# Optimization experiments

Measured on AMD Instinct MI355X. Metric: run time of the kernel, lower is better.

The kernel has to match this reference:

```python
import jax, jax.numpy as jnp
import numpy as np

DIL = 64  # dilation; l_wing = (filter_sz-1)*dil = 64
B, R, C, D, S, T = 8, 128, 128, 128, 256, 16384


def _xavier(key, shape, fan_in, fan_out):
    a = np.sqrt(6.0 / (fan_in + fan_out)).astype(np.float32)
    return jax.random.uniform(key, shape, jnp.float32, -a, a)


def setup_inputs() -> dict:
    key = jax.random.key(0)
    ks = jax.random.split(key, 10)
    return {
        'x': jax.random.normal(ks[0], (B, R, T), jnp.float32),
        'cond': jax.random.normal(ks[1], (B, C, T), jnp.float32),
        # dilated convs, kernel size 2: weight (out=D, in=R, k=2), bias (D,)
        'w_sig': _xavier(ks[2], (D, R, 2), R * 2, D * 2),
        'b_sig': jnp.zeros((D,), jnp.float32),
        'w_gate': _xavier(ks[3], (D, R, 2), R * 2, D * 2),
        'b_gate': jnp.zeros((D,), jnp.float32),
        # 1x1 cond projections (no bias): (D, C)
        'w_psig': _xavier(ks[4], (D, C), C, D),
        'w_pgate': _xavier(ks[5], (D, C), C, D),
        # 1x1 residual / skip projections (no bias)
        'w_res': _xavier(ks[6], (R, D), D, R),
        'w_skp': _xavier(ks[7], (S, D), D, S),
    }


def reference(x, cond, w_sig, b_sig, w_gate, b_gate, w_psig, w_pgate, w_res, w_skp):
    d = DIL
    # dilated kernel-size-2 conv1d expressed as two shifted 1x1 contractions
    x0 = x[:, :, :-d]   # tap at offset 0, length T-d
    x1 = x[:, :, d:]    # tap at offset d, length T-d
    c = cond[:, :, d:]  # cond_lead = l_wing = d in full mode
    filt = (jnp.einsum('brt,dr->bdt', x0, w_sig[:, :, 0])
            + jnp.einsum('brt,dr->bdt', x1, w_sig[:, :, 1])
            + jnp.einsum('bct,dc->bdt', c, w_psig)
            + b_sig[None, :, None])
    gate = (jnp.einsum('brt,dr->bdt', x0, w_gate[:, :, 0])
            + jnp.einsum('brt,dr->bdt', x1, w_gate[:, :, 1])
            + jnp.einsum('bct,dc->bdt', c, w_pgate)
            + b_gate[None, :, None])
    z = jnp.tanh(filt) * jax.nn.sigmoid(gate)   # (B, D, T-d)
    sig = jnp.einsum('bdt,rd->brt', z, w_res) + x1  # residual add, (B, R, T-d)
    skp = jnp.einsum('bdt,sd->bst', z, w_skp)       # skip_lead = 0, (B, S, T-d)
    return (sig, skp)
```

## Files before the change

kernel.cpp:

```cpp
#include <hip/hip_runtime.h>
#include <math.h>

#define NB   8
#define NR   128
#define NC   128
#define ND   128
#define NS   256
#define NT   16384
#define DILC 64
#define TTV  16320
#define TBW  48
#define NTILE 340

typedef __attribute__((ext_vector_type(8))) short bf16x8;
typedef __attribute__((ext_vector_type(4))) float f32x4;

typedef unsigned short ushort_t;
typedef unsigned int   uint_t;

__device__ __forceinline__ ushort_t f2bf(float f) {
    uint_t u = __float_as_uint(f);
    u += 0x7FFFu + ((u >> 16) & 1u);
    return (ushort_t)(u >> 16);
}
__device__ __forceinline__ float bf2f(ushort_t h) {
    return __uint_as_float(((uint_t)h) << 16);
}

#define SWZ(t) ((((t) ^ ((t) >> 2)) & 7) << 4)

__global__ void pack_w1(const float* __restrict__ w_sig, const float* __restrict__ w_gate,
                        const float* __restrict__ w_psig, const float* __restrict__ w_pgate,
                        ushort_t* __restrict__ Wh, ushort_t* __restrict__ Wl) {
    int idx = blockIdx.x * 256 + threadIdx.x;
    int frag = idx >> 9, e = idx & 511;
    int rr = e >> 5, kk = e & 31;
    int m = frag & 15, ks = frag >> 4;
    int prow = m * 16 + rr;
    int d = prow >> 1, g = prow & 1;
    int k = ks * 32 + kk;
    const float* wa = g ? w_gate : w_sig;
    const float* wp = g ? w_pgate : w_psig;
    float v;
    if (k < 128)      v = wa[d * 256 + k * 2 + 0];
    else if (k < 256) v = wa[d * 256 + (k - 128) * 2 + 1];
    else              v = wp[d * 128 + (k - 256)];
    ushort_t h = f2bf(v);
    Wh[idx] = h;
    Wl[idx] = f2bf(v - bf2f(h));
}

__global__ void pack_w2(const float* __restrict__ w_res, const float* __restrict__ w_skp,
                        ushort_t* __restrict__ Wh, ushort_t* __restrict__ Wl) {
    int idx = blockIdx.x * 256 + threadIdx.x;
    int frag = idx >> 9, e = idx & 511;
    int rr = e >> 5, kk = e & 31;
    int m = frag >> 2, ks = frag & 3;
    int row = m * 16 + rr;
    int k = ks * 32 + kk;
    float v = (row < 128) ? w_res[row * 128 + k] : w_skp[(row - 128) * 128 + k];
    ushort_t h = f2bf(v);
    Wh[idx] = h;
    Wl[idx] = f2bf(v - bf2f(h));
}

__global__ __launch_bounds__(256, 2)
void fused_mfma(const float* __restrict__ x, const float* __restrict__ cond,
                const ushort_t* __restrict__ W1h, const ushort_t* __restrict__ W1l,
                const ushort_t* __restrict__ W2h, const ushort_t* __restrict__ W2l,
                const float* __restrict__ b_sig, const float* __restrict__ b_gate,
                float* __restrict__ out) {
    __shared__ ushort_t xsh[112 * 128];
    __shared__ ushort_t xsl[112 * 128];
    __shared__ ushort_t csh[48 * 128];
    __shared__ ushort_t csl[48 * 128];

    const int tid  = threadIdx.x;
    const int lane = tid & 63;
    const int w    = tid >> 6;
    const int t0   = blockIdx.x * TBW;
    const int b    = blockIdx.y;

    {
        const float* xb = x + (size_t)b * NR * NT;
#pragma unroll
        for (int it = 0; it < 16; ++it) {
            int idx = it * 256 + tid;
            int r = idx >> 5, c4 = idx & 31;
            if (c4 < 28) {
                float4 v = *reinterpret_cast<const float4*>(xb + (size_t)r * NT + t0 + c4 * 4);
                float vv[4] = {v.x, v.y, v.z, v.w};
#pragma unroll
                for (int j = 0; j < 4; ++j) {
                    int tt = c4 * 4 + j;
                    ushort_t h = f2bf(vv[j]);
                    ushort_t l = f2bf(vv[j] - bf2f(h));
                    int byte = ((tt << 8) + (r << 1)) ^ SWZ(tt);
                    *(ushort_t*)((char*)xsh + byte) = h;
                    *(ushort_t*)((char*)xsl + byte) = l;
                }
            }
        }
    }
    {
        const float* cb = cond + (size_t)b * NC * NT + DILC;
#pragma unroll
        for (int it = 0; it < 8; ++it) {
            int idx = it * 256 + tid;
            int r = idx >> 4, c4 = idx & 15;
            if (c4 < 12) {
                float4 v = *reinterpret_cast<const float4*>(cb + (size_t)r * NT + t0 + c4 * 4);
                float vv[4] = {v.x, v.y, v.z, v.w};
#pragma unroll
                for (int j = 0; j < 4; ++j) {
                    int tt = c4 * 4 + j;
                    ushort_t h = f2bf(vv[j]);
                    ushort_t l = f2bf(vv[j] - bf2f(h));
                    int byte = ((tt << 8) + (r << 1)) ^ SWZ(tt);
                    *(ushort_t*)((char*)csh + byte) = h;
                    *(ushort_t*)((char*)csl + byte) = l;
                }
            }
        }
    }
    __syncthreads();

    const int tcol = lane & 15;
    const int koct = lane >> 4;
    const int aoff = tcol * 32 + koct * 8;

    f32x4 acc[4][3];
#pragma unroll
    for (int m = 0; m < 4; ++m)
#pragma unroll
        for (int n = 0; n < 3; ++n) acc[m][n] = (f32x4){0.f, 0.f, 0.f, 0.f};

#pragma unroll
    for (int seg = 0; seg < 3; ++seg) {
#pragma unroll
        for (int k2 = 0; k2 < 4; ++k2) {
            const int ks = seg * 4 + k2;
            bf16x8 ah[4], al[4];
#pragma unroll
            for (int m = 0; m < 4; ++m) {
                int f = ks * 16 + (w * 4 + m);
                ah[m] = *reinterpret_cast<const bf16x8*>(W1h + f * 512 + aoff);
                al[m] = *reinterpret_cast<const bf16x8*>(W1l + f * 512 + aoff);
            }
            bf16x8 bh[3], bl[3];
            const int kin = k2 * 32 + koct * 8;
            const ushort_t* ph = (seg == 2) ? csh : xsh;
            const ushort_t* pl = (seg == 2) ? csl : xsl;
            const int tadd = (seg == 1) ? 64 : 0;
#pragma unroll
            for (int n = 0; n < 3; ++n) {
                int t = n * 16 + tcol + tadd;
                int byte = ((t << 8) + (kin << 1)) ^ SWZ(t);
                bh[n] = *reinterpret_cast<const bf16x8*>((const char*)ph + byte);
                bl[n] = *reinterpret_cast<const bf16x8*>((const char*)pl + byte);
            }
#pragma unroll
            for (int m = 0; m < 4; ++m)
#pragma unroll
                for (int n = 0; n < 3; ++n) {
                    acc[m][n] = __builtin_amdgcn_mfma_f32_16x16x32_bf16(ah[m], bh[n], acc[m][n], 0, 0, 0);
                    acc[m][n] = __builtin_amdgcn_mfma_f32_16x16x32_bf16(ah[m], bl[n], acc[m][n], 0, 0, 0);
                    acc[m][n] = __builtin_amdgcn_mfma_f32_16x16x32_bf16(al[m], bh[n], acc[m][n], 0, 0, 0);
                }
        }
    }

    __syncthreads();

#pragma unroll
    for (int m = 0; m < 4; ++m) {
        int d0 = (w * 4 + m) * 8 + koct * 2;
        float bs0 = b_sig[d0], bg0 = b_gate[d0];
        float bs1 = b_sig[d0 + 1], bg1 = b_gate[d0 + 1];
#pragma unroll
        for (int n = 0; n < 3; ++n) {
            int t = n * 16 + tcol;
            float f0 = acc[m][n][0] + bs0, g0 = acc[m][n][1] + bg0;
            float f1 = acc[m][n][2] + bs1, g1 = acc[m][n][3] + bg1;
            float e0 = __expf(2.f * f0), e1 = __expf(2.f * f1);
            float th0 = 1.f - 2.f * __builtin_amdgcn_rcpf(e0 + 1.f);
            float th1 = 1.f - 2.f * __builtin_amdgcn_rcpf(e1 + 1.f);
            float sg0 = __builtin_amdgcn_rcpf(1.f + __expf(-g0));
            float sg1 = __builtin_amdgcn_rcpf(1.f + __expf(-g1));
            float z0 = th0 * sg0, z1 = th1 * sg1;
            ushort_t h0 = f2bf(z0), h1 = f2bf(z1);
            ushort_t l0 = f2bf(z0 - bf2f(h0)), l1 = f2bf(z1 - bf2f(h1));
            int byte = ((t << 8) + (d0 << 1)) ^ SWZ(t);
            *(uint_t*)((char*)csh + byte) = (uint_t)h0 | ((uint_t)h1 << 16);
            *(uint_t*)((char*)csl + byte) = (uint_t)l0 | ((uint_t)l1 << 16);
        }
    }
    __syncthreads();

    f32x4 acc2[6][3];
#pragma unroll
    for (int m = 0; m < 6; ++m)
#pragma unroll
        for (int n = 0; n < 3; ++n) acc2[m][n] = (f32x4){0.f, 0.f, 0.f, 0.f};

#pragma unroll
    for (int ks = 0; ks < 4; ++ks) {
        bf16x8 ah[6], al[6];
#pragma unroll
        for (int m = 0; m < 6; ++m) {
            int f = (w * 6 + m) * 4 + ks;
            ah[m] = *reinterpret_cast<const bf16x8*>(W2h + f * 512 + aoff);
            al[m] = *reinterpret_cast<const bf16x8*>(W2l + f * 512 + aoff);
        }
        bf16x8 bh[3], bl[3];
        const int kin = ks * 32 + koct * 8;
#pragma unroll
        for (int n = 0; n < 3; ++n) {
            int t = n * 16 + tcol;
            int byte = ((t << 8) + (kin << 1)) ^ SWZ(t);
            bh[n] = *reinterpret_cast<const bf16x8*>((const char*)csh + byte);
            bl[n] = *reinterpret_cast<const bf16x8*>((const char*)csl + byte);
        }
#pragma unroll
        for (int m = 0; m < 6; ++m)
#pragma unroll
            for (int n = 0; n < 3; ++n) {
                acc2[m][n] = __builtin_amdgcn_mfma_f32_16x16x32_bf16(ah[m], bh[n], acc2[m][n], 0, 0, 0);
                acc2[m][n] = __builtin_amdgcn_mfma_f32_16x16x32_bf16(ah[m], bl[n], acc2[m][n], 0, 0, 0);
                acc2[m][n] = __builtin_amdgcn_mfma_f32_16x16x32_bf16(al[m], bh[n], acc2[m][n], 0, 0, 0);
            }
    }

    const float* xres   = x + (size_t)b * NR * NT + t0 + DILC;
    float* sig_out = out + (size_t)b * NR * TTV + t0;
    float* skp_out = out + (size_t)NB * NR * TTV + (size_t)b * NS * TTV + t0;
#pragma unroll
    for (int m = 0; m < 6; ++m) {
        int prow = (w * 6 + m) * 16 + koct * 4;
#pragma unroll
        for (int n = 0; n < 3; ++n) {
            int t = n * 16 + tcol;
#pragma unroll
            for (int q = 0; q < 4; ++q) {
                int row = prow + q;
                float v = acc2[m][n][q];
                if (row < 128) {
                    v += xres[(size_t)row * NT + t];
                    sig_out[(size_t)row * TTV + t] = v;
                } else {
                    skp_out[(size_t)(row - 128) * TTV + t] = v;
                }
            }
        }
    }
}

extern "C" void kernel_launch(void* const* d_in, const int* in_sizes, int n_in,
                              void* d_out, int out_size, void* d_ws, size_t ws_size,
                              hipStream_t stream) {
    const float* x       = (const float*)d_in[0];
    const float* cond    = (const float*)d_in[1];
    const float* w_sig   = (const float*)d_in[2];
    const float* b_sig   = (const float*)d_in[3];
    const float* w_gate  = (const float*)d_in[4];
    const float* b_gate  = (const float*)d_in[5];
    const float* w_psig  = (const float*)d_in[6];
    const float* w_pgate = (const float*)d_in[7];
    const float* w_res   = (const float*)d_in[8];
    const float* w_skp   = (const float*)d_in[9];
    float* out = (float*)d_out;

    ushort_t* W1h = (ushort_t*)d_ws;
    ushort_t* W1l = W1h + 98304;
    ushort_t* W2h = W1l + 98304;
    ushort_t* W2l = W2h + 49152;
    if (ws_size < (size_t)(2 * (98304 + 49152)) * sizeof(ushort_t)) return;

    pack_w1<<<384, 256, 0, stream>>>(w_sig, w_gate, w_psig, w_pgate, W1h, W1l);
    pack_w2<<<192, 256, 0, stream>>>(w_res, w_skp, W2h, W2l);

    dim3 grid(NTILE, NB);
    fused_mfma<<<grid, 256, 0, stream>>>(x, cond, W1h, W1l, W2h, W2l, b_sig, b_gate, out);
}
```

Measured before the change: 527.3 us.

## Shrink time tile, drop redundant x staging, double-buffer weight loads, reuse LDS residual

The time tile shrinks from 48 to 32 columns. Only the two tap windows of x are staged into LDS, so the unused middle columns are no longer loaded. Occupancy rises to 3 blocks per SM, and the grid becomes 1D with batch as the fastest-varying index. Weight fragments for both GEMMs are software-pipelined with double buffering. The second GEMM runs per output row block to cut register pressure, and the residual x1 is rebuilt from the bf16 hi/lo copies in LDS instead of a second global read. The residual reconstructed from hi+lo bf16 carries slightly less than full fp32 precision.

Result: faster. 465.1 us (-11.8%).

```diff
diff --git a/kernel.cpp b/kernel.cpp
--- a/kernel.cpp
+++ b/kernel.cpp
@@ -9,8 +9,8 @@
 #define NT   16384
 #define DILC 64
 #define TTV  16320
-#define TBW  48
-#define NTILE 340
+#define TBW  32
+#define NTILE 510
 
 typedef __attribute__((ext_vector_type(8))) short bf16x8;
 typedef __attribute__((ext_vector_type(4))) float f32x4;
@@ -64,62 +64,62 @@
     Wl[idx] = f2bf(v - bf2f(h));
 }
 
-__global__ __launch_bounds__(256, 2)
+__global__ __launch_bounds__(256, 3)
 void fused_mfma(const float* __restrict__ x, const float* __restrict__ cond,
                 const ushort_t* __restrict__ W1h, const ushort_t* __restrict__ W1l,
                 const ushort_t* __restrict__ W2h, const ushort_t* __restrict__ W2l,
                 const float* __restrict__ b_sig, const float* __restrict__ b_gate,
                 float* __restrict__ out) {
-    __shared__ ushort_t xsh[112 * 128];
-    __shared__ ushort_t xsl[112 * 128];
-    __shared__ ushort_t csh[48 * 128];
-    __shared__ ushort_t csl[48 * 128];
+    __shared__ ushort_t xsh[64 * 128];
+    __shared__ ushort_t xsl[64 * 128];
+    __shared__ ushort_t csh[32 * 128];
+    __shared__ ushort_t csl[32 * 128];
 
     const int tid  = threadIdx.x;
     const int lane = tid & 63;
     const int w    = tid >> 6;
-    const int t0   = blockIdx.x * TBW;
-    const int b    = blockIdx.y;
+
+    const int s    = blockIdx.x;
+    const int b    = s & 7;
+    const int tile = s >> 3;
+    const int t0   = tile * TBW;
 
     {
         const float* xb = x + (size_t)b * NR * NT;
-#pragma unroll
-        for (int it = 0; it < 16; ++it) {
-            int idx = it * 256 + tid;
-            int r = idx >> 5, c4 = idx & 31;
-            if (c4 < 28) {
-                float4 v = *reinterpret_cast<const float4*>(xb + (size_t)r * NT + t0 + c4 * 4);
-                float vv[4] = {v.x, v.y, v.z, v.w};
-#pragma unroll
-                for (int j = 0; j < 4; ++j) {
-                    int tt = c4 * 4 + j;
-                    ushort_t h = f2bf(vv[j]);
-                    ushort_t l = f2bf(vv[j] - bf2f(h));
-                    int byte = ((tt << 8) + (r << 1)) ^ SWZ(tt);
-                    *(ushort_t*)((char*)xsh + byte) = h;
-                    *(ushort_t*)((char*)xsl + byte) = l;
-                }
-            }
-        }
-    }
-    {
-        const float* cb = cond + (size_t)b * NC * NT + DILC;
 #pragma unroll
         for (int it = 0; it < 8; ++it) {
             int idx = it * 256 + tid;
             int r = idx >> 4, c4 = idx & 15;
-            if (c4 < 12) {
-                float4 v = *reinterpret_cast<const float4*>(cb + (size_t)r * NT + t0 + c4 * 4);
-                float vv[4] = {v.x, v.y, v.z, v.w};
-#pragma unroll
-                for (int j = 0; j < 4; ++j) {
-                    int tt = c4 * 4 + j;
-                    ushort_t h = f2bf(vv[j]);
-                    ushort_t l = f2bf(vv[j] - bf2f(h));
-                    int byte = ((tt << 8) + (r << 1)) ^ SWZ(tt);
-                    *(ushort_t*)((char*)csh + byte) = h;
-                    *(ushort_t*)((char*)csl + byte) = l;
-                }
+            int gcol = (c4 < 8) ? c4 * 4 : c4 * 4 + 32;
+            float4 v = *reinterpret_cast<const float4*>(xb + (size_t)r * NT + t0 + gcol);
+            float vv[4] = {v.x, v.y, v.z, v.w};
+#pragma unroll
+            for (int j = 0; j < 4; ++j) {
+                int c = c4 * 4 + j;
+                ushort_t h = f2bf(vv[j]);
+                ushort_t l = f2bf(vv[j] - bf2f(h));
+                int byte = ((c << 8) + (r << 1)) ^ SWZ(c);
+                *(ushort_t*)((char*)xsh + byte) = h;
+                *(ushort_t*)((char*)xsl + byte) = l;
+            }
+        }
+    }
+    {
+        const float* cb = cond + (size_t)b * NC * NT + DILC;
+#pragma unroll
+        for (int it = 0; it < 4; ++it) {
+            int idx = it * 256 + tid;
+            int r = idx >> 3, c4 = idx & 7;
+            float4 v = *reinterpret_cast<const float4*>(cb + (size_t)r * NT + t0 + c4 * 4);
+            float vv[4] = {v.x, v.y, v.z, v.w};
+#pragma unroll
+            for (int j = 0; j < 4; ++j) {
+                int c = c4 * 4 + j;
+                ushort_t h = f2bf(vv[j]);
+                ushort_t l = f2bf(vv[j] - bf2f(h));
+                int byte = ((c << 8) + (r << 1)) ^ SWZ(c);
+                *(ushort_t*)((char*)csh + byte) = h;
+                *(ushort_t*)((char*)csl + byte) = l;
             }
         }
     }
@@ -129,45 +129,48 @@
     const int koct = lane >> 4;
     const int aoff = tcol * 32 + koct * 8;
 
-    f32x4 acc[4][3];
+    f32x4 acc[4][2];
 #pragma unroll
     for (int m = 0; m < 4; ++m)
 #pragma unroll
-        for (int n = 0; n < 3; ++n) acc[m][n] = (f32x4){0.f, 0.f, 0.f, 0.f};
-
-#pragma unroll
-    for (int seg = 0; seg < 3; ++seg) {
-#pragma unroll
-        for (int k2 = 0; k2 < 4; ++k2) {
-            const int ks = seg * 4 + k2;
-            bf16x8 ah[4], al[4];
-#pragma unroll
-            for (int m = 0; m < 4; ++m) {
-                int f = ks * 16 + (w * 4 + m);
-                ah[m] = *reinterpret_cast<const bf16x8*>(W1h + f * 512 + aoff);
-                al[m] = *reinterpret_cast<const bf16x8*>(W1l + f * 512 + aoff);
-            }
-            bf16x8 bh[3], bl[3];
-            const int kin = k2 * 32 + koct * 8;
-            const ushort_t* ph = (seg == 2) ? csh : xsh;
-            const ushort_t* pl = (seg == 2) ? csl : xsl;
-            const int tadd = (seg == 1) ? 64 : 0;
-#pragma unroll
-            for (int n = 0; n < 3; ++n) {
-                int t = n * 16 + tcol + tadd;
-                int byte = ((t << 8) + (kin << 1)) ^ SWZ(t);
-                bh[n] = *reinterpret_cast<const bf16x8*>((const char*)ph + byte);
-                bl[n] = *reinterpret_cast<const bf16x8*>((const char*)pl + byte);
-            }
-#pragma unroll
-            for (int m = 0; m < 4; ++m)
-#pragma unroll
-                for (int n = 0; n < 3; ++n) {
-                    acc[m][n] = __builtin_amdgcn_mfma_f32_16x16x32_bf16(ah[m], bh[n], acc[m][n], 0, 0, 0);
-                    acc[m][n] = __builtin_amdgcn_mfma_f32_16x16x32_bf16(ah[m], bl[n], acc[m][n], 0, 0, 0);
-                    acc[m][n] = __builtin_amdgcn_mfma_f32_16x16x32_bf16(al[m], bh[n], acc[m][n], 0, 0, 0);
-                }
-        }
+        for (int n = 0; n < 2; ++n) acc[m][n] = (f32x4){0.f, 0.f, 0.f, 0.f};
+
+    bf16x8 pah[2][4], pal[2][4];
+#define LOADA1(BUFI, KSV)                                                        \
+    {                                                                            \
+        _Pragma("unroll") for (int m_ = 0; m_ < 4; ++m_) {                       \
+            int f_ = (KSV) * 16 + (w * 4 + m_);                                  \
+            pah[BUFI][m_] = *reinterpret_cast<const bf16x8*>(W1h + f_ * 512 + aoff); \
+            pal[BUFI][m_] = *reinterpret_cast<const bf16x8*>(W1l + f_ * 512 + aoff); \
+        }                                                                        \
+    }
+
+    LOADA1(0, 0);
+#pragma unroll
+    for (int ks = 0; ks < 12; ++ks) {
+        const int cur = ks & 1, nxt = cur ^ 1;
+        if (ks < 11) LOADA1(nxt, ks + 1);
+        const int seg = ks >> 2, k2 = ks & 3;
+        const int kin = k2 * 32 + koct * 8;
+        const ushort_t* ph = (seg == 2) ? csh : xsh;
+        const ushort_t* pl = (seg == 2) ? csl : xsl;
+        const int cbase = (seg == 1) ? 32 : 0;
+        bf16x8 bh[2], bl[2];
+#pragma unroll
+        for (int n = 0; n < 2; ++n) {
+            int c = cbase + n * 16 + tcol;
+            int byte = ((c << 8) + (kin << 1)) ^ SWZ(c);
+            bh[n] = *reinterpret_cast<const bf16x8*>((const char*)ph + byte);
+            bl[n] = *reinterpret_cast<const bf16x8*>((const char*)pl + byte);
+        }
+#pragma unroll
+        for (int m = 0; m < 4; ++m)
+#pragma unroll
+            for (int n = 0; n < 2; ++n) {
+                acc[m][n] = __builtin_amdgcn_mfma_f32_16x16x32_bf16(pah[cur][m], bh[n], acc[m][n], 0, 0, 0);
+                acc[m][n] = __builtin_amdgcn_mfma_f32_16x16x32_bf16(pah[cur][m], bl[n], acc[m][n], 0, 0, 0);
+                acc[m][n] = __builtin_amdgcn_mfma_f32_16x16x32_bf16(pal[cur][m], bh[n], acc[m][n], 0, 0, 0);
+            }
     }
 
     __syncthreads();
@@ -178,7 +181,7 @@
         float bs0 = b_sig[d0], bg0 = b_gate[d0];
         float bs1 = b_sig[d0 + 1], bg1 = b_gate[d0 + 1];
 #pragma unroll
-        for (int n = 0; n < 3; ++n) {
+        for (int n = 0; n < 2; ++n) {
             int t = n * 16 + tcol;
             float f0 = acc[m][n][0] + bs0, g0 = acc[m][n][1] + bg0;
             float f1 = acc[m][n][2] + bs1, g1 = acc[m][n][3] + bg1;
@@ -197,56 +200,55 @@
     }
     __syncthreads();
 
-    f32x4 acc2[6][3];
-#pragma unroll
-    for (int m = 0; m < 6; ++m)
-#pragma unroll
-        for (int n = 0; n < 3; ++n) acc2[m][n] = (f32x4){0.f, 0.f, 0.f, 0.f};
-
-#pragma unroll
-    for (int ks = 0; ks < 4; ++ks) {
-        bf16x8 ah[6], al[6];
-#pragma unroll
-        for (int m = 0; m < 6; ++m) {
-            int f = (w * 6 + m) * 4 + ks;
-            ah[m] = *reinterpret_cast<const bf16x8*>(W2h + f * 512 + aoff);
-            al[m] = *reinterpret_cast<const bf16x8*>(W2l + f * 512 + aoff);
-        }
-        bf16x8 bh[3], bl[3];
-        const int kin = ks * 32 + koct * 8;
-#pragma unroll
-        for (int n = 0; n < 3; ++n) {
-            int t = n * 16 + tcol;
-            int byte = ((t << 8) + (kin << 1)) ^ SWZ(t);
-            bh[n] = *reinterpret_cast<const bf16x8*>((const char*)csh + byte);
-            bl[n] = *reinterpret_cast<const bf16x8*>((const char*)csl + byte);
-        }
-#pragma unroll
-        for (int m = 0; m < 6; ++m)
-#pragma unroll
-            for (int n = 0; n < 3; ++n) {
-                acc2[m][n] = __builtin_amdgcn_mfma_f32_16x16x32_bf16(ah[m], bh[n], acc2[m][n], 0, 0, 0);
-                acc2[m][n] = __builtin_amdgcn_mfma_f32_16x16x32_bf16(ah[m], bl[n], acc2[m][n], 0, 0, 0);
-                acc2[m][n] = __builtin_amdgcn_mfma_f32_16x16x32_bf16(al[m], bh[n], acc2[m][n], 0, 0, 0);
-            }
-    }
-
-    const float* xres   = x + (size_t)b * NR * NT + t0 + DILC;
     float* sig_out = out + (size_t)b * NR * TTV + t0;
     float* skp_out = out + (size_t)NB * NR * TTV + (size_t)b * NS * TTV + t0;
+
+    bf16x8 qah[2][4], qal[2][4];
+#define LOADA2(BUFI, MV)                                                         \
+    {                                                                            \
+        _Pragma("unroll") for (int ks_ = 0; ks_ < 4; ++ks_) {                    \
+            int f_ = (w * 6 + (MV)) * 4 + ks_;                                   \
+            qah[BUFI][ks_] = *reinterpret_cast<const bf16x8*>(W2h + f_ * 512 + aoff); \
+            qal[BUFI][ks_] = *reinterpret_cast<const bf16x8*>(W2l + f_ * 512 + aoff); \
+        }                                                                        \
+    }
+
+    LOADA2(0, 0);
 #pragma unroll
     for (int m = 0; m < 6; ++m) {
+        const int cur = m & 1, nxt = cur ^ 1;
+        if (m < 5) LOADA2(nxt, m + 1);
+        f32x4 a2[2];
+        a2[0] = (f32x4){0.f, 0.f, 0.f, 0.f};
+        a2[1] = (f32x4){0.f, 0.f, 0.f, 0.f};
+#pragma unroll
+        for (int ks = 0; ks < 4; ++ks) {
+            const int kin = ks * 32 + koct * 8;
+#pragma unroll
+            for (int n = 0; n < 2; ++n) {
+                int t = n * 16 + tcol;
+                int byte = ((t << 8) + (kin << 1)) ^ SWZ(t);
+                bf16x8 bh = *reinterpret_cast<const bf16x8*>((const char*)csh + byte);
+                bf16x8 bl = *reinterpret_cast<const bf16x8*>((const char*)csl + byte);
+                a2[n] = __builtin_amdgcn_mfma_f32_16x16x32_bf16(qah[cur][ks], bh, a2[n], 0, 0, 0);
+                a2[n] = __builtin_amdgcn_mfma_f32_16x16x32_bf16(qah[cur][ks], bl, a2[n], 0, 0, 0);
+                a2[n] = __builtin_amdgcn_mfma_f32_16x16x32_bf16(qal[cur][ks], bh, a2[n], 0, 0, 0);
+            }
+        }
         int prow = (w * 6 + m) * 16 + koct * 4;
 #pragma unroll
-        for (int n = 0; n < 3; ++n) {
+        for (int n = 0; n < 2; ++n) {
             int t = n * 16 + tcol;
 #pragma unroll
             for (int q = 0; q < 4; ++q) {
                 int row = prow + q;
-                float v = acc2[m][n][q];
-                if (row < 128) {
-                    v += xres[(size_t)row * NT + t];
-                    sig_out[(size_t)row * TTV + t] = v;
+                float v = a2[n][q];
+                if (w * 6 + m < 8) {
+                    int c = 32 + t;
+                    int byte = ((c << 8) + (row << 1)) ^ SWZ(c);
+                    float x1v = bf2f(*(const ushort_t*)((const char*)xsh + byte))
+                              + bf2f(*(const ushort_t*)((const char*)xsl + byte));
+                    sig_out[(size_t)row * TTV + t] = v + x1v;
                 } else {
                     skp_out[(size_t)(row - 128) * TTV + t] = v;
                 }
@@ -279,6 +281,5 @@
     pack_w1<<<384, 256, 0, stream>>>(w_sig, w_gate, w_psig, w_pgate, W1h, W1l);
     pack_w2<<<192, 256, 0, stream>>>(w_res, w_skp, W2h, W2l);
 
-    dim3 grid(NTILE, NB);
-    fused_mfma<<<grid, 256, 0, stream>>>(x, cond, W1h, W1l, W2h, W2l, b_sig, b_gate, out);
-}
+    fused_mfma<<<NTILE * NB, 256, 0, stream>>>(x, cond, W1h, W1l, W2h, W2l, b_sig, b_gate, out);
+}
```
